# Kernel tuning notes

Measured on AMD Instinct MI355X. Metric: run time of the kernel, lower is better.

The kernel has to match this reference:

```python
import jax, jax.numpy as jnp
import numpy as np

N_HEADS = 16
ROPE_DIMS = 64


def _rope_tables(T, rd):
    # freqs: 1 / 10000^(arange(0, rd, 2)/rd), shape [rd//2]
    freqs = 1.0 / (10000.0 ** (np.arange(0, rd, 2, dtype=np.float32) / np.float32(rd)))
    ang = np.outer(np.arange(T, dtype=np.float32), freqs)  # [T, rd//2]
    return jnp.asarray(np.cos(ang)), jnp.asarray(np.sin(ang))


def _apply_rope(x, cos, sin, rd):
    # x: [B, H, T, D]; rotate-half style on first rd dims
    x_rope, x_pass = x[..., :rd], x[..., rd:]
    x1, x2 = x_rope[..., : rd // 2], x_rope[..., rd // 2 :]
    c = cos[None, None]  # [1,1,T,rd//2]
    s = sin[None, None]
    x_rot = jnp.concatenate([x1 * c - x2 * s, x2 * c + x1 * s], axis=-1)
    return jnp.concatenate([x_rot, x_pass], axis=-1)


def setup_inputs() -> dict:
    key = jax.random.key(0)
    k1, k2, k3 = jax.random.split(key, 3)
    B, T, C = 32, 512, 2048
    x = jax.random.normal(k1, (B, T, C), dtype=jnp.float32)
    w_qkv = jax.random.normal(k2, (3 * C, C), dtype=jnp.float32) * 0.02
    w_out = jax.random.normal(k3, (C, C), dtype=jnp.float32) * 0.02
    return {"x": x, "w_qkv": w_qkv, "w_out": w_out}


def reference(x, w_qkv, w_out):
    B, T, C = x.shape
    H = N_HEADS
    D = C // H
    # fused QKV projection: F.linear(x, w) = x @ w.T
    qkv = jnp.einsum('btc,fc->btf', x, w_qkv).reshape(B, T, 3, H, D)
    q = jnp.transpose(qkv[:, :, 0], (0, 2, 1, 3))  # [B,H,T,D]
    k = jnp.transpose(qkv[:, :, 1], (0, 2, 1, 3))
    v = jnp.transpose(qkv[:, :, 2], (0, 2, 1, 3))
    cos, sin = _rope_tables(T, ROPE_DIMS)
    q = _apply_rope(q, cos, sin, ROPE_DIMS)
    k = _apply_rope(k, cos, sin, ROPE_DIMS)
    # causal SDPA
    scale = 1.0 / jnp.sqrt(jnp.asarray(D, dtype=x.dtype))
    scores = jnp.einsum('bhqd,bhkd->bhqk', q, k) * scale
    causal = jnp.tril(jnp.ones((T, T), dtype=bool))
    scores = jnp.where(causal[None, None], scores, jnp.finfo(scores.dtype).min)
    attn = jax.nn.softmax(scores, axis=-1)
    y = jnp.einsum('bhqk,bhkd->bhqd', attn, v)
    y = jnp.transpose(y, (0, 2, 1, 3)).reshape(B, T, C)
    return jnp.einsum('btc,fc->btf', y, w_out)
```

## Files before the change

kernel.cpp:

```cpp
#include <hip/hip_runtime.h>


typedef __bf16 bf16x8 __attribute__((ext_vector_type(8)));
typedef float floatx4 __attribute__((ext_vector_type(4)));

__device__ __forceinline__ unsigned short f2bf(float f) {
  union { float f; unsigned u; } v; v.f = f;
  unsigned r = v.u + 0x7FFFu + ((v.u >> 16) & 1u);
  return (unsigned short)(r >> 16);
}
__device__ __forceinline__ float bf2f(unsigned short h) {
  union { unsigned u; float f; } v; v.u = ((unsigned)h) << 16; return v.f;
}

__device__ __forceinline__ void load_lds16(const void* g, void* l) {
  __builtin_amdgcn_global_load_lds((__attribute__((address_space(1))) void*)g,
                                   (__attribute__((address_space(3))) void*)l,
                                   16, 0, 0);
}

#define BARRIER() asm volatile("s_barrier" ::: "memory")
#define VMCNT6()  asm volatile("s_waitcnt vmcnt(6)" ::: "memory")
#define VMCNT0()  asm volatile("s_waitcnt vmcnt(0)" ::: "memory")

__global__ void rope_tables(float* __restrict__ cost, float* __restrict__ sint) {
  int i = blockIdx.x * 256 + threadIdx.x;
  if (i >= 512 * 32) return;
  int t = i >> 5, f = i & 31;
  float e = -(float)(2 * f) / 64.0f;
  float freq = powf(10000.0f, e);
  float ang = (float)t * freq;
  cost[i] = cosf(ang);
  sint[i] = sinf(ang);
}

__global__ void cast_bf16(const float* __restrict__ in,
                          unsigned short* __restrict__ out, int n8) {
  int i = blockIdx.x * 256 + threadIdx.x;
  if (i >= n8) return;
  float4 a = ((const float4*)in)[2 * i];
  float4 b = ((const float4*)in)[2 * i + 1];
  union { uint4 v; unsigned short u[8]; } o;
  o.u[0] = f2bf(a.x); o.u[1] = f2bf(a.y); o.u[2] = f2bf(a.z); o.u[3] = f2bf(a.w);
  o.u[4] = f2bf(b.x); o.u[5] = f2bf(b.y); o.u[6] = f2bf(b.z); o.u[7] = f2bf(b.w);
  ((uint4*)out)[i] = o.v;
}

template <int OUT_BF16>
__global__ __launch_bounds__(512, 2) void gemm256(
    const unsigned short* __restrict__ A, const unsigned short* __restrict__ Bt,
    void* __restrict__ Cout, int M, int N, int K) {
  __shared__ __align__(16) unsigned short As[2][16384];
  __shared__ __align__(16) unsigned short Bs[2][16384];

  const int tid = threadIdx.x;
  const int nbx = gridDim.x;
  const int nwg = nbx * gridDim.y;
  const int lin = blockIdx.y * nbx + blockIdx.x;
  const int swz = (lin & 7) * (nwg >> 3) + (lin >> 3);
  const int bm = swz / nbx, bn = swz % nbx;

  const int w = tid >> 6, l = tid & 63;
  const int wm = w >> 2, wn = w & 3;
  const int quad = l >> 4, cl = l & 15;
  const int xs0 = ((0 + quad) ^ (cl & 7)) << 3;
  const int xs1 = ((4 + quad) ^ (cl & 7)) << 3;
  const int aoff = (wm * 128 + cl) * 64;
  const int boff = (wn * 64 + cl) * 64;

  const int srow = tid >> 3;
  const int lc = (tid & 7) ^ (srow & 7);
  const unsigned short* Ag = A + (size_t)(bm * 256 + srow) * K + lc * 8;
  const unsigned short* Bg = Bt + (size_t)(bn * 256 + srow) * K + lc * 8;

  auto stageA = [&](int q, int h, int k0) {
    const unsigned short* src = Ag + (size_t)(h * 128) * K + k0;
    unsigned short* dst = &As[q][0] + h * 8192 + tid * 8;
    load_lds16(src, dst);
    load_lds16(src + (size_t)64 * K, dst + 4096);
  };
  auto stageB = [&](int q, int h, int k0) {
    const unsigned short* src = Bg + (size_t)(h * 128) * K + k0;
    unsigned short* dst = &Bs[q][0] + h * 8192 + tid * 8;
    load_lds16(src, dst);
    load_lds16(src + (size_t)64 * K, dst + 4096);
  };

  floatx4 acc[8][4] = {};
  const int NT = K >> 6;

  stageA(0, 0, 0);  stageA(0, 1, 0);  stageB(0, 0, 0);  stageB(0, 1, 0);
  stageA(1, 0, 64); stageA(1, 1, 64); stageB(1, 0, 64);
  VMCNT6();
  BARRIER();

  for (int t = 0; t < NT; ++t) {
    const int q = t & 1;
    const unsigned short* pA = &As[q][0] + aoff;
    const unsigned short* pB = &Bs[q][0] + boff;
    const int k2 = (t + 2) << 6;
    const bool s2 = (t + 2) < NT;

    bf16x8 a0[4][2], a1[4][2], b0[2][2], b1[2][2];
#pragma unroll
    for (int mi = 0; mi < 4; ++mi) {
      a0[mi][0] = *(const bf16x8*)(pA + mi * 1024 + xs0);
      a0[mi][1] = *(const bf16x8*)(pA + mi * 1024 + xs1);
    }
#pragma unroll
    for (int ni = 0; ni < 2; ++ni) {
      b0[ni][0] = *(const bf16x8*)(pB + ni * 1024 + xs0);
      b0[ni][1] = *(const bf16x8*)(pB + ni * 1024 + xs1);
    }
    if (t + 1 < NT) stageB(q ^ 1, 1, (t + 1) << 6);
    BARRIER();
    __builtin_amdgcn_s_setprio(1);
#pragma unroll
    for (int mi = 0; mi < 4; ++mi)
#pragma unroll
      for (int ni = 0; ni < 2; ++ni)
#pragma unroll
        for (int ks = 0; ks < 2; ++ks)
          acc[mi][ni] = __builtin_amdgcn_mfma_f32_16x16x32_bf16(
              a0[mi][ks], b0[ni][ks], acc[mi][ni], 0, 0, 0);
    __builtin_amdgcn_s_setprio(0);
    BARRIER();
#pragma unroll
    for (int mi = 0; mi < 4; ++mi) {
      a1[mi][0] = *(const bf16x8*)(pA + (mi + 4) * 1024 + xs0);
      a1[mi][1] = *(const bf16x8*)(pA + (mi + 4) * 1024 + xs1);
    }
    BARRIER();
    __builtin_amdgcn_s_setprio(1);
#pragma unroll
    for (int mi = 0; mi < 4; ++mi)
#pragma unroll
      for (int ni = 0; ni < 2; ++ni)
#pragma unroll
        for (int ks = 0; ks < 2; ++ks)
          acc[mi + 4][ni] = __builtin_amdgcn_mfma_f32_16x16x32_bf16(
              a1[mi][ks], b0[ni][ks], acc[mi + 4][ni], 0, 0, 0);
    __builtin_amdgcn_s_setprio(0);
    BARRIER();
#pragma unroll
    for (int ni = 0; ni < 2; ++ni) {
      b1[ni][0] = *(const bf16x8*)(pB + (ni + 2) * 1024 + xs0);
      b1[ni][1] = *(const bf16x8*)(pB + (ni + 2) * 1024 + xs1);
    }
    if (s2) stageA(q, 0, k2);
    BARRIER();
    __builtin_amdgcn_s_setprio(1);
#pragma unroll
    for (int mi = 0; mi < 4; ++mi)
#pragma unroll
      for (int ni = 0; ni < 2; ++ni)
#pragma unroll
        for (int ks = 0; ks < 2; ++ks)
          acc[mi + 4][ni + 2] = __builtin_amdgcn_mfma_f32_16x16x32_bf16(
              a1[mi][ks], b1[ni][ks], acc[mi + 4][ni + 2], 0, 0, 0);
    __builtin_amdgcn_s_setprio(0);
    BARRIER();
    if (s2) { stageA(q, 1, k2); stageB(q, 0, k2); }
    BARRIER();
    __builtin_amdgcn_s_setprio(1);
#pragma unroll
    for (int mi = 0; mi < 4; ++mi)
#pragma unroll
      for (int ni = 0; ni < 2; ++ni)
#pragma unroll
        for (int ks = 0; ks < 2; ++ks)
          acc[mi][ni + 2] = __builtin_amdgcn_mfma_f32_16x16x32_bf16(
              a0[mi][ks], b1[ni][ks], acc[mi][ni + 2], 0, 0, 0);
    __builtin_amdgcn_s_setprio(0);
    if (t < NT - 2) { VMCNT6(); } else { VMCNT0(); }
    BARRIER();
  }

#pragma unroll
  for (int mi = 0; mi < 8; ++mi)
#pragma unroll
    for (int ni = 0; ni < 4; ++ni)
#pragma unroll
      for (int r = 0; r < 4; ++r) {
        const int gm = bm * 256 + wm * 128 + mi * 16 + quad * 4 + r;
        const int gn = bn * 256 + wn * 64 + ni * 16 + cl;
        const float v = acc[mi][ni][r];
        if (OUT_BF16)
          ((unsigned short*)Cout)[(size_t)gm * N + gn] = f2bf(v);
        else
          ((float*)Cout)[(size_t)gm * N + gn] = v;
      }
}

__global__ __launch_bounds__(256) void attn_kernel(
    const unsigned short* __restrict__ qkv, const float* __restrict__ cost,
    const float* __restrict__ sint, unsigned short* __restrict__ y) {
  __shared__ __align__(16) unsigned short Qs[64][136];
  __shared__ __align__(16) unsigned short Ks[64][136];
  __shared__ __align__(16) unsigned short VTs[128][64];
  __shared__ __align__(16) unsigned short Ps[4][16][72];

  const int bh = blockIdx.x, qt = blockIdx.y;
  const int b = bh >> 4, h = bh & 15;
  const int tid = threadIdx.x, w = tid >> 6, l = tid & 63;
  const int quad = l >> 4, cl = l & 15;
  const float scale = 0.08838834764831845f * 1.4426950408889634f;

  {
    const int r = tid >> 2, j = tid & 3;
    const int tg = qt * 64 + r;
    const unsigned short* qrow = qkv + (size_t)(b * 512 + tg) * 6144 + h * 128;
    union { uint4 v; unsigned short u[8]; } c1, c2, p1, p2, o1, o2, o3, o4;
    c1.v = *(const uint4*)(qrow + j * 8);
    c2.v = *(const uint4*)(qrow + j * 8 + 32);
    p1.v = *(const uint4*)(qrow + 64 + j * 16);
    p2.v = *(const uint4*)(qrow + 64 + j * 16 + 8);
#pragma unroll
    for (int jj = 0; jj < 8; ++jj) {
      int d = j * 8 + jj;
      float c = cost[tg * 32 + d], s = sint[tg * 32 + d];
      float x1 = bf2f(c1.u[jj]), x2 = bf2f(c2.u[jj]);
      o1.u[jj] = f2bf((x1 * c - x2 * s) * scale);
      o2.u[jj] = f2bf((x2 * c + x1 * s) * scale);
      o3.u[jj] = f2bf(bf2f(p1.u[jj]) * scale);
      o4.u[jj] = f2bf(bf2f(p2.u[jj]) * scale);
    }
    *(uint4*)&Qs[r][j * 8]          = o1.v;
    *(uint4*)&Qs[r][j * 8 + 32]     = o2.v;
    *(uint4*)&Qs[r][64 + j * 16]     = o3.v;
    *(uint4*)&Qs[r][64 + j * 16 + 8] = o4.v;
  }

  floatx4 o[8] = {};
  float m_i[4] = {-__builtin_inff(), -__builtin_inff(), -__builtin_inff(),
                  -__builtin_inff()};
  float l_i[4] = {0.f, 0.f, 0.f, 0.f};

  for (int ktile = 0; ktile <= qt; ++ktile) {
    __syncthreads();
    {
      const int r = tid >> 2, j = tid & 3;
      const int tg = ktile * 64 + r;
      const unsigned short* krow =
          qkv + (size_t)(b * 512 + tg) * 6144 + 2048 + h * 128;
      union { uint4 v; unsigned short u[8]; } c1, c2, p1, p2, o1, o2;
      c1.v = *(const uint4*)(krow + j * 8);
      c2.v = *(const uint4*)(krow + j * 8 + 32);
      p1.v = *(const uint4*)(krow + 64 + j * 16);
      p2.v = *(const uint4*)(krow + 64 + j * 16 + 8);
#pragma unroll
      for (int jj = 0; jj < 8; ++jj) {
        int d = j * 8 + jj;
        float c = cost[tg * 32 + d], s = sint[tg * 32 + d];
        float x1 = bf2f(c1.u[jj]), x2 = bf2f(c2.u[jj]);
        o1.u[jj] = f2bf(x1 * c - x2 * s);
        o2.u[jj] = f2bf(x2 * c + x1 * s);
      }
      *(uint4*)&Ks[r][j * 8]          = o1.v;
      *(uint4*)&Ks[r][j * 8 + 32]     = o2.v;
      *(uint4*)&Ks[r][64 + j * 16]     = p1.v;
      *(uint4*)&Ks[r][64 + j * 16 + 8] = p2.v;
    }
    {
      const int rowg = tid >> 5;
      const int colg = tid & 31;
      const int kk0 = rowg * 8, d0 = colg * 4;
      const unsigned short* vbase = qkv +
          (size_t)(b * 512 + ktile * 64 + kk0) * 6144 + 4096 + h * 128 + d0;
      uint2 rv[8];
#pragma unroll
      for (int rr = 0; rr < 8; ++rr)
        rv[rr] = *(const uint2*)(vbase + (size_t)rr * 6144);
#pragma unroll
      for (int c = 0; c < 4; ++c) {
        const int d = d0 + c;
        unsigned out[4];
#pragma unroll
        for (int p = 0; p < 4; ++p) {
          unsigned ua = ((const unsigned*)&rv[2 * p])[c >> 1];
          unsigned ub = ((const unsigned*)&rv[2 * p + 1])[c >> 1];
          unsigned lo = (c & 1) ? (ua >> 16) : (ua & 0xffffu);
          unsigned hi = (c & 1) ? (ub >> 16) : (ub & 0xffffu);
          out[p] = lo | (hi << 16);
        }
        *(uint4*)&VTs[d][(rowg ^ (d & 7)) << 3] = *(uint4*)out;
      }
    }
    __syncthreads();

    floatx4 s[4] = {};
#pragma unroll
    for (int kc = 0; kc < 4; ++kc) {
      bf16x8 aq = *(const bf16x8*)(&Qs[w * 16 + cl][kc * 32 + quad * 8]);
#pragma unroll
      for (int nt = 0; nt < 4; ++nt) {
        bf16x8 bk = *(const bf16x8*)(&Ks[nt * 16 + cl][kc * 32 + quad * 8]);
        s[nt] = __builtin_amdgcn_mfma_f32_16x16x32_bf16(aq, bk, s[nt], 0, 0, 0);
      }
    }
    if (ktile == qt) {
#pragma unroll
      for (int nt = 0; nt < 4; ++nt)
#pragma unroll
        for (int r = 0; r < 4; ++r) {
          int qrow_l = w * 16 + quad * 4 + r;
          int kcol_l = nt * 16 + cl;
          if (kcol_l > qrow_l) s[nt][r] = -__builtin_inff();
        }
    }
#pragma unroll
    for (int r = 0; r < 4; ++r) {
      float mx = fmaxf(fmaxf(s[0][r], s[1][r]), fmaxf(s[2][r], s[3][r]));
      mx = fmaxf(mx, __shfl_xor(mx, 1));
      mx = fmaxf(mx, __shfl_xor(mx, 2));
      mx = fmaxf(mx, __shfl_xor(mx, 4));
      mx = fmaxf(mx, __shfl_xor(mx, 8));
      float mn = fmaxf(m_i[r], mx);
      float a = exp2f(m_i[r] - mn);
      float rs = 0.f;
#pragma unroll
      for (int nt = 0; nt < 4; ++nt) {
        float p = exp2f(s[nt][r] - mn);
        s[nt][r] = p;
        rs += p;
      }
      rs += __shfl_xor(rs, 1);
      rs += __shfl_xor(rs, 2);
      rs += __shfl_xor(rs, 4);
      rs += __shfl_xor(rs, 8);
      l_i[r] = l_i[r] * a + rs;
      m_i[r] = mn;
#pragma unroll
      for (int nt2 = 0; nt2 < 8; ++nt2) o[nt2][r] *= a;
#pragma unroll
      for (int nt = 0; nt < 4; ++nt)
        Ps[w][quad * 4 + r][nt * 16 + cl] = f2bf(s[nt][r]);
    }
    __syncthreads();

#pragma unroll
    for (int kc2 = 0; kc2 < 2; ++kc2) {
      bf16x8 ap = *(const bf16x8*)(&Ps[w][cl][kc2 * 32 + quad * 8]);
#pragma unroll
      for (int nt2 = 0; nt2 < 8; ++nt2) {
        bf16x8 bv = *(const bf16x8*)(
            &VTs[nt2 * 16 + cl][((kc2 * 4 + quad) ^ (cl & 7)) << 3]);
        o[nt2] = __builtin_amdgcn_mfma_f32_16x16x32_bf16(ap, bv, o[nt2], 0, 0, 0);
      }
    }
  }

#pragma unroll
  for (int r = 0; r < 4; ++r) {
    float inv = 1.0f / l_i[r];
    size_t row =
        (size_t)(b * 512 + qt * 64 + w * 16 + quad * 4 + r) * 2048 + h * 128;
#pragma unroll
    for (int nt2 = 0; nt2 < 8; ++nt2)
      y[row + nt2 * 16 + cl] = f2bf(o[nt2][r] * inv);
  }
}

extern "C" void kernel_launch(void* const* d_in, const int* in_sizes, int n_in,
                              void* d_out, int out_size, void* d_ws,
                              size_t ws_size, hipStream_t stream) {
  const float* x = (const float*)d_in[0];
  const float* wqkv = (const float*)d_in[1];
  const float* wout = (const float*)d_in[2];
  float* out = (float*)d_out;

  char* ws = (char*)d_ws;
  float* cost = (float*)ws;            ws += (size_t)512 * 32 * 4;
  float* sint = (float*)ws;            ws += (size_t)512 * 32 * 4;
  unsigned short* xb = (unsigned short*)ws;    ws += (size_t)16384 * 2048 * 2;
  unsigned short* wqkvb = (unsigned short*)ws; ws += (size_t)6144 * 2048 * 2;
  unsigned short* woutb = (unsigned short*)ws; ws += (size_t)2048 * 2048 * 2;
  unsigned short* qkvb = (unsigned short*)ws;  ws += (size_t)16384 * 6144 * 2;
  unsigned short* yb = (unsigned short*)ws;    ws += (size_t)16384 * 2048 * 2;

  rope_tables<<<dim3(64), dim3(256), 0, stream>>>(cost, sint);
  cast_bf16<<<dim3(16384), dim3(256), 0, stream>>>(x, xb, 33554432 / 8);
  cast_bf16<<<dim3(6144), dim3(256), 0, stream>>>(wqkv, wqkvb, 12582912 / 8);
  cast_bf16<<<dim3(2048), dim3(256), 0, stream>>>(wout, woutb, 4194304 / 8);
  gemm256<1><<<dim3(24, 64), dim3(512), 0, stream>>>(xb, wqkvb, (void*)qkvb,
                                                     16384, 6144, 2048);
  attn_kernel<<<dim3(512, 8), dim3(256), 0, stream>>>(qkvb, cost, sint, yb);
  gemm256<0><<<dim3(8, 64), dim3(512), 0, stream>>>(yb, woutb, (void*)out,
                                                    16384, 2048, 2048);
}
```

Baseline: 948.8 us.

## Precompute RoPE in separate pass and double-buffer K/V tiles in attention

Moves RoPE rotation and Q scaling out of the attention kernel into a separate in-place pass over the QKV buffer. The attention kernel then keeps Q fragments in registers, stages K directly into swizzled LDS with async global-to-LDS loads, and double-buffers K and V so the next tile's loads overlap the current tile's MFMA work. It also drops one barrier per iteration and raises wave priority around the MFMA sections. The cost is an extra kernel that reads and writes the Q/K halves of QKV, plus twice the LDS for K/V buffers, which may lower occupancy.

```diff
diff --git a/kernel.cpp b/kernel.cpp
--- a/kernel.cpp
+++ b/kernel.cpp
@@ -44,6 +44,58 @@
   o.u[0] = f2bf(a.x); o.u[1] = f2bf(a.y); o.u[2] = f2bf(a.z); o.u[3] = f2bf(a.w);
   o.u[4] = f2bf(b.x); o.u[5] = f2bf(b.y); o.u[6] = f2bf(b.z); o.u[7] = f2bf(b.w);
   ((uint4*)out)[i] = o.v;
+}
+
+__global__ __launch_bounds__(256) void rope_apply(
+    unsigned short* __restrict__ qkv, const float* __restrict__ cost,
+    const float* __restrict__ sint) {
+  const int idx = blockIdx.x * 256 + threadIdx.x;
+  const int tok = idx >> 4, h = idx & 15;
+  const int t = tok & 511;
+  const float scale = 0.08838834764831845f * 1.4426950408889634f;
+  unsigned short* qrow = qkv + (size_t)tok * 6144 + h * 128;
+  unsigned short* krow = qrow + 2048;
+
+  float cs[32], sn[32];
+#pragma unroll
+  for (int j = 0; j < 8; ++j) {
+    *(float4*)&cs[j * 4] = *(const float4*)&cost[t * 32 + j * 4];
+    *(float4*)&sn[j * 4] = *(const float4*)&sint[t * 32 + j * 4];
+  }
+  union u32x4 { uint4 v[4]; unsigned short u[32]; };
+  u32x4 q1, q2, k1, k2, o1, o2, o3, o4;
+#pragma unroll
+  for (int j = 0; j < 4; ++j) {
+    q1.v[j] = *(const uint4*)(qrow + j * 8);
+    q2.v[j] = *(const uint4*)(qrow + 32 + j * 8);
+    k1.v[j] = *(const uint4*)(krow + j * 8);
+    k2.v[j] = *(const uint4*)(krow + 32 + j * 8);
+  }
+#pragma unroll
+  for (int d = 0; d < 32; ++d) {
+    float c = cs[d], s = sn[d];
+    float qx1 = bf2f(q1.u[d]), qx2 = bf2f(q2.u[d]);
+    o1.u[d] = f2bf((qx1 * c - qx2 * s) * scale);
+    o2.u[d] = f2bf((qx2 * c + qx1 * s) * scale);
+    float kx1 = bf2f(k1.u[d]), kx2 = bf2f(k2.u[d]);
+    o3.u[d] = f2bf(kx1 * c - kx2 * s);
+    o4.u[d] = f2bf(kx2 * c + kx1 * s);
+  }
+#pragma unroll
+  for (int j = 0; j < 4; ++j) {
+    *(uint4*)(qrow + j * 8)      = o1.v[j];
+    *(uint4*)(qrow + 32 + j * 8) = o2.v[j];
+    *(uint4*)(krow + j * 8)      = o3.v[j];
+    *(uint4*)(krow + 32 + j * 8) = o4.v[j];
+  }
+#pragma unroll
+  for (int j = 0; j < 8; ++j) {
+    union { uint4 v; unsigned short u[8]; } p, po;
+    p.v = *(const uint4*)(qrow + 64 + j * 8);
+#pragma unroll
+    for (int jj = 0; jj < 8; ++jj) po.u[jj] = f2bf(bf2f(p.u[jj]) * scale);
+    *(uint4*)(qrow + 64 + j * 8) = po.v;
+  }
 }
 
 template <int OUT_BF16>
@@ -193,112 +245,96 @@
 }
 
 __global__ __launch_bounds__(256) void attn_kernel(
-    const unsigned short* __restrict__ qkv, const float* __restrict__ cost,
-    const float* __restrict__ sint, unsigned short* __restrict__ y) {
-  __shared__ __align__(16) unsigned short Qs[64][136];
-  __shared__ __align__(16) unsigned short Ks[64][136];
-  __shared__ __align__(16) unsigned short VTs[128][64];
+    const unsigned short* __restrict__ qkv, unsigned short* __restrict__ y) {
+  __shared__ __align__(16) unsigned short Ks[2][64][128];
+  __shared__ __align__(16) unsigned short VTs[2][128][64];
   __shared__ __align__(16) unsigned short Ps[4][16][72];
 
   const int bh = blockIdx.x, qt = blockIdx.y;
   const int b = bh >> 4, h = bh & 15;
   const int tid = threadIdx.x, w = tid >> 6, l = tid & 63;
   const int quad = l >> 4, cl = l & 15;
-  const float scale = 0.08838834764831845f * 1.4426950408889634f;
-
+
+  bf16x8 aq[4];
   {
-    const int r = tid >> 2, j = tid & 3;
-    const int tg = qt * 64 + r;
-    const unsigned short* qrow = qkv + (size_t)(b * 512 + tg) * 6144 + h * 128;
-    union { uint4 v; unsigned short u[8]; } c1, c2, p1, p2, o1, o2, o3, o4;
-    c1.v = *(const uint4*)(qrow + j * 8);
-    c2.v = *(const uint4*)(qrow + j * 8 + 32);
-    p1.v = *(const uint4*)(qrow + 64 + j * 16);
-    p2.v = *(const uint4*)(qrow + 64 + j * 16 + 8);
-#pragma unroll
-    for (int jj = 0; jj < 8; ++jj) {
-      int d = j * 8 + jj;
-      float c = cost[tg * 32 + d], s = sint[tg * 32 + d];
-      float x1 = bf2f(c1.u[jj]), x2 = bf2f(c2.u[jj]);
-      o1.u[jj] = f2bf((x1 * c - x2 * s) * scale);
-      o2.u[jj] = f2bf((x2 * c + x1 * s) * scale);
-      o3.u[jj] = f2bf(bf2f(p1.u[jj]) * scale);
-      o4.u[jj] = f2bf(bf2f(p2.u[jj]) * scale);
-    }
-    *(uint4*)&Qs[r][j * 8]          = o1.v;
-    *(uint4*)&Qs[r][j * 8 + 32]     = o2.v;
-    *(uint4*)&Qs[r][64 + j * 16]     = o3.v;
-    *(uint4*)&Qs[r][64 + j * 16 + 8] = o4.v;
-  }
+    const unsigned short* qrow =
+        qkv + (size_t)(b * 512 + qt * 64 + w * 16 + cl) * 6144 + h * 128 +
+        quad * 8;
+#pragma unroll
+    for (int kc = 0; kc < 4; ++kc) aq[kc] = *(const bf16x8*)(qrow + kc * 32);
+  }
+
+  const int krow = tid >> 4;
+  const int kslot = tid & 15;
+  const int kchunk = (kslot & 8) | ((kslot & 7) ^ (krow & 7));
+  const unsigned short* kgbase =
+      qkv + (size_t)(b * 512) * 6144 + 2048 + h * 128 + kchunk * 8;
+  auto stageK = [&](int buf, int kt) {
+#pragma unroll
+    for (int slab = 0; slab < 4; ++slab) {
+      const unsigned short* src =
+          kgbase + (size_t)(kt * 64 + slab * 16 + krow) * 6144;
+      load_lds16(src, &Ks[buf][0][0] + slab * 2048 + tid * 8);
+    }
+  };
+
+  const int rowg = tid >> 5, colg = tid & 31;
+  const unsigned short* vgbase =
+      qkv + (size_t)(b * 512 + rowg * 8) * 6144 + 4096 + h * 128 + colg * 4;
+  uint2 rv[8];
+  auto loadV = [&](int kt) {
+    const unsigned short* p = vgbase + (size_t)(kt * 64) * 6144;
+#pragma unroll
+    for (int rr = 0; rr < 8; ++rr) rv[rr] = *(const uint2*)(p + (size_t)rr * 6144);
+  };
+  auto writeV = [&](int buf) {
+#pragma unroll
+    for (int c = 0; c < 4; ++c) {
+      const int d = colg * 4 + c;
+      unsigned out[4];
+#pragma unroll
+      for (int p = 0; p < 4; ++p) {
+        unsigned ua = ((const unsigned*)&rv[2 * p])[c >> 1];
+        unsigned ub = ((const unsigned*)&rv[2 * p + 1])[c >> 1];
+        unsigned lo = (c & 1) ? (ua >> 16) : (ua & 0xffffu);
+        unsigned hi = (c & 1) ? (ub >> 16) : (ub & 0xffffu);
+        out[p] = lo | (hi << 16);
+      }
+      *(uint4*)&VTs[buf][d][(rowg ^ (d & 7)) << 3] = *(uint4*)out;
+    }
+  };
 
   floatx4 o[8] = {};
   float m_i[4] = {-__builtin_inff(), -__builtin_inff(), -__builtin_inff(),
                   -__builtin_inff()};
   float l_i[4] = {0.f, 0.f, 0.f, 0.f};
 
-  for (int ktile = 0; ktile <= qt; ++ktile) {
-    __syncthreads();
-    {
-      const int r = tid >> 2, j = tid & 3;
-      const int tg = ktile * 64 + r;
-      const unsigned short* krow =
-          qkv + (size_t)(b * 512 + tg) * 6144 + 2048 + h * 128;
-      union { uint4 v; unsigned short u[8]; } c1, c2, p1, p2, o1, o2;
-      c1.v = *(const uint4*)(krow + j * 8);
-      c2.v = *(const uint4*)(krow + j * 8 + 32);
-      p1.v = *(const uint4*)(krow + 64 + j * 16);
-      p2.v = *(const uint4*)(krow + 64 + j * 16 + 8);
-#pragma unroll
-      for (int jj = 0; jj < 8; ++jj) {
-        int d = j * 8 + jj;
-        float c = cost[tg * 32 + d], s = sint[tg * 32 + d];
-        float x1 = bf2f(c1.u[jj]), x2 = bf2f(c2.u[jj]);
-        o1.u[jj] = f2bf(x1 * c - x2 * s);
-        o2.u[jj] = f2bf(x2 * c + x1 * s);
+  stageK(0, 0);
+  loadV(0);
+  VMCNT0();
+  writeV(0);
+  __syncthreads();
+
+  for (int kt = 0; kt <= qt; ++kt) {
+    const int qb = kt & 1;
+    const bool more = (kt < qt);
+    if (more) { stageK(qb ^ 1, kt + 1); loadV(kt + 1); }
+
+    floatx4 s[4] = {};
+    __builtin_amdgcn_s_setprio(1);
+#pragma unroll
+    for (int kc = 0; kc < 4; ++kc) {
+#pragma unroll
+      for (int nt = 0; nt < 4; ++nt) {
+        const int row = nt * 16 + cl;
+        const int c = kc * 4 + quad;
+        const int sc = (c & 8) | ((c & 7) ^ (row & 7));
+        bf16x8 bk = *(const bf16x8*)(&Ks[qb][row][sc * 8]);
+        s[nt] = __builtin_amdgcn_mfma_f32_16x16x32_bf16(aq[kc], bk, s[nt], 0, 0, 0);
       }
-      *(uint4*)&Ks[r][j * 8]          = o1.v;
-      *(uint4*)&Ks[r][j * 8 + 32]     = o2.v;
-      *(uint4*)&Ks[r][64 + j * 16]     = p1.v;
-      *(uint4*)&Ks[r][64 + j * 16 + 8] = p2.v;
-    }
-    {
-      const int rowg = tid >> 5;
-      const int colg = tid & 31;
-      const int kk0 = rowg * 8, d0 = colg * 4;
-      const unsigned short* vbase = qkv +
-          (size_t)(b * 512 + ktile * 64 + kk0) * 6144 + 4096 + h * 128 + d0;
-      uint2 rv[8];
-#pragma unroll
-      for (int rr = 0; rr < 8; ++rr)
-        rv[rr] = *(const uint2*)(vbase + (size_t)rr * 6144);
-#pragma unroll
-      for (int c = 0; c < 4; ++c) {
-        const int d = d0 + c;
-        unsigned out[4];
-#pragma unroll
-        for (int p = 0; p < 4; ++p) {
-          unsigned ua = ((const unsigned*)&rv[2 * p])[c >> 1];
-          unsigned ub = ((const unsigned*)&rv[2 * p + 1])[c >> 1];
-          unsigned lo = (c & 1) ? (ua >> 16) : (ua & 0xffffu);
-          unsigned hi = (c & 1) ? (ub >> 16) : (ub & 0xffffu);
-          out[p] = lo | (hi << 16);
-        }
-        *(uint4*)&VTs[d][(rowg ^ (d & 7)) << 3] = *(uint4*)out;
-      }
-    }
-    __syncthreads();
-
-    floatx4 s[4] = {};
-#pragma unroll
-    for (int kc = 0; kc < 4; ++kc) {
-      bf16x8 aq = *(const bf16x8*)(&Qs[w * 16 + cl][kc * 32 + quad * 8]);
-#pragma unroll
-      for (int nt = 0; nt < 4; ++nt) {
-        bf16x8 bk = *(const bf16x8*)(&Ks[nt * 16 + cl][kc * 32 + quad * 8]);
-        s[nt] = __builtin_amdgcn_mfma_f32_16x16x32_bf16(aq, bk, s[nt], 0, 0, 0);
-      }
-    }
-    if (ktile == qt) {
+    }
+    __builtin_amdgcn_s_setprio(0);
+    if (kt == qt) {
 #pragma unroll
       for (int nt = 0; nt < 4; ++nt)
 #pragma unroll
@@ -336,18 +372,25 @@
       for (int nt = 0; nt < 4; ++nt)
         Ps[w][quad * 4 + r][nt * 16 + cl] = f2bf(s[nt][r]);
     }
-    __syncthreads();
-
+
+    __builtin_amdgcn_s_setprio(1);
 #pragma unroll
     for (int kc2 = 0; kc2 < 2; ++kc2) {
       bf16x8 ap = *(const bf16x8*)(&Ps[w][cl][kc2 * 32 + quad * 8]);
 #pragma unroll
       for (int nt2 = 0; nt2 < 8; ++nt2) {
         bf16x8 bv = *(const bf16x8*)(
-            &VTs[nt2 * 16 + cl][((kc2 * 4 + quad) ^ (cl & 7)) << 3]);
+            &VTs[qb][nt2 * 16 + cl][((kc2 * 4 + quad) ^ (cl & 7)) << 3]);
         o[nt2] = __builtin_amdgcn_mfma_f32_16x16x32_bf16(ap, bv, o[nt2], 0, 0, 0);
       }
     }
+    __builtin_amdgcn_s_setprio(0);
+
+    if (more) {
+      VMCNT0();
+      writeV(qb ^ 1);
+    }
+    __syncthreads();
   }
 
 #pragma unroll
@@ -384,7 +427,8 @@
   cast_bf16<<<dim3(2048), dim3(256), 0, stream>>>(wout, woutb, 4194304 / 8);
   gemm256<1><<<dim3(24, 64), dim3(512), 0, stream>>>(xb, wqkvb, (void*)qkvb,
                                                      16384, 6144, 2048);
-  attn_kernel<<<dim3(512, 8), dim3(256), 0, stream>>>(qkvb, cost, sint, yb);
+  rope_apply<<<dim3(1024), dim3(256), 0, stream>>>(qkvb, cost, sint);
+  attn_kernel<<<dim3(512, 8), dim3(256), 0, stream>>>(qkvb, yb);
   gemm256<0><<<dim3(8, 64), dim3(512), 0, stream>>>(yb, woutb, (void*)out,
                                                     16384, 2048, 2048);
 }
```

Result: slower. 1.027 ms (+8.3%).
